# Optimization experiments

Hardware: AMD Instinct MI355X
Metric: run time of the kernel (lower is better)

Reference implementation:

```python
import jax, jax.numpy as jnp
import numpy as np

B, S, D = 4, 1024, 2048
H, KVH, HD = 32, 8, 64
N_REP = H // KVH  # 4
ROPE_THETA = 1000000.0


def _rope_tables(seq_len, head_dim, theta):
    inv_freq = 1.0 / (theta ** (np.arange(0, head_dim, 2, dtype=np.float32) / head_dim))
    t = np.arange(seq_len, dtype=np.float32)
    freqs = np.outer(t, inv_freq)                      # (S, HD/2)
    emb = np.concatenate([freqs, freqs], axis=-1)      # (S, HD)
    return jnp.asarray(np.cos(emb)), jnp.asarray(np.sin(emb))


def setup_inputs() -> dict:
    key = jax.random.key(0)
    kx, kq, kk, kv, ko = jax.random.split(key, 5)
    cos, sin = _rope_tables(S, HD, ROPE_THETA)
    s = 0.02
    return {
        "x": jax.random.normal(kx, (B, S, D), jnp.float32),
        "cos": cos,
        "sin": sin,
        "Wq": jax.random.normal(kq, (D, H * HD), jnp.float32) * s,
        "Wk": jax.random.normal(kk, (D, KVH * HD), jnp.float32) * s,
        "Wv": jax.random.normal(kv, (D, KVH * HD), jnp.float32) * s,
        "Wo": jax.random.normal(ko, (H * HD, D), jnp.float32) * s,
    }


def _rotate_half(t):
    t1, t2 = jnp.split(t, 2, axis=-1)
    return jnp.concatenate([-t2, t1], axis=-1)


def reference(x, cos, sin, Wq, Wk, Wv, Wo):
    # projections
    q = (x @ Wq).reshape(B, S, H, HD)      # (b, s, h, d)
    k = (x @ Wk).reshape(B, S, KVH, HD)
    v = (x @ Wv).reshape(B, S, KVH, HD)

    # RoPE: cos/sin (s, d) broadcast over heads (unsqueeze_dim=1 -> (s,1,d))
    c = cos[:, None, :]
    sn = sin[:, None, :]
    q = q * c + _rotate_half(q) * sn
    k = k * c + _rotate_half(k) * sn

    # GQA attention without physically repeating KV:
    # q grouped as (b, kvh, n_rep, s, d); repeat_kv '(h r)' maps q head g*n_rep+r -> kv head g
    qg = q.transpose(0, 2, 1, 3).reshape(B, KVH, N_REP, S, HD)
    kt = k.transpose(0, 2, 1, 3)  # (b, kvh, s, d)
    vt = v.transpose(0, 2, 1, 3)

    scale = 1.0 / jnp.sqrt(jnp.asarray(HD, x.dtype))
    scores = jnp.einsum('bgrqd,bgkd->bgrqk', qg, kt) * scale  # (b, kvh, rep, s, s)
    probs = jax.nn.softmax(scores, axis=-1)
    out = jnp.einsum('bgrqk,bgkd->bgrqd', probs, vt)           # (b, kvh, rep, s, d)

    out = out.reshape(B, H, S, HD).transpose(0, 2, 1, 3).reshape(B, S, H * HD)
    return out @ Wo
```

## Files before the change

kernel.cpp:

```cpp
#include <hip/hip_runtime.h>

typedef unsigned short u16;
typedef __attribute__((ext_vector_type(8))) __bf16 bf16x8;
typedef __attribute__((ext_vector_type(4))) _Float16 f16x4;
typedef __attribute__((ext_vector_type(8))) _Float16 f16x8;
typedef __attribute__((ext_vector_type(4))) float f32x4;

#define BB 4
#define SS 1024
#define DD 2048
#define HH 32
#define KVHN 8
#define HDIM 64

__device__ __forceinline__ u16 f2b(float f) {
    union { float f; unsigned u; } v; v.f = f;
    unsigned r = v.u + 0x7FFFu + ((v.u >> 16) & 1u);
    return (u16)(r >> 16);
}
__device__ __forceinline__ float b2f(u16 h) {
    union { unsigned u; float f; } v; v.u = ((unsigned)h) << 16; return v.f;
}

__device__ __forceinline__ f32x4 mfma16(bf16x8 a, bf16x8 b, f32x4 c) {
    return __builtin_amdgcn_mfma_f32_16x16x32_bf16(a, b, c, 0, 0, 0);
}
__device__ __forceinline__ f32x4 mfma16h(f16x8 a, f16x8 b, f32x4 c) {
    return __builtin_amdgcn_mfma_f32_16x16x32_f16(a, b, c, 0, 0, 0);
}

__device__ __forceinline__ void async_cp16(const void* g, void* l) {
    __builtin_amdgcn_global_load_lds((__attribute__((address_space(1))) void*)g,
                                     (__attribute__((address_space(3))) void*)l,
                                     16, 0, 0);
}

__device__ __forceinline__ void block_sync() {
    asm volatile("" ::: "memory");
    __builtin_amdgcn_s_barrier();
    asm volatile("" ::: "memory");
}

__device__ __forceinline__ f16x8 pack8_f16(const float* p) {
    union { unsigned u[4]; f16x8 v; } pu;
    pu.u[0] = __builtin_bit_cast(unsigned, __builtin_amdgcn_cvt_pkrtz(p[0], p[1]));
    pu.u[1] = __builtin_bit_cast(unsigned, __builtin_amdgcn_cvt_pkrtz(p[2], p[3]));
    pu.u[2] = __builtin_bit_cast(unsigned, __builtin_amdgcn_cvt_pkrtz(p[4], p[5]));
    pu.u[3] = __builtin_bit_cast(unsigned, __builtin_amdgcn_cvt_pkrtz(p[6], p[7]));
    return pu.v;
}

__global__ __launch_bounds__(256) void cast_x_kernel(const float* __restrict__ x,
                                                     u16* __restrict__ xb) {
    int i = (blockIdx.x * 256 + threadIdx.x) * 4;
    float4 v = *(const float4*)(x + i);
    unsigned r0 = (unsigned)f2b(v.x) | ((unsigned)f2b(v.y) << 16);
    unsigned r1 = (unsigned)f2b(v.z) | ((unsigned)f2b(v.w) << 16);
    *(uint2*)(xb + i) = make_uint2(r0, r1);
}

__global__ __launch_bounds__(256) void wtrans_all_kernel(const float* __restrict__ Wq,
                                                         const float* __restrict__ Wk,
                                                         const float* __restrict__ Wv,
                                                         const float* __restrict__ Wo,
                                                         u16* __restrict__ Wqkvt,
                                                         u16* __restrict__ Wot) {
    __shared__ float tile[32][33];
    int z = blockIdx.z;
    const float* W = (z == 0) ? Wq : (z == 1) ? Wk : (z == 2) ? Wv : Wo;
    int N = (z == 1 || z == 2) ? 512 : 2048;
    int n_off = (z == 1) ? 2048 : (z == 2) ? 2560 : 0;
    u16* Wt = (z == 3) ? Wot : Wqkvt;
    int n0 = blockIdx.x * 32;
    if (n0 >= N) return;
    int k0 = blockIdx.y * 32;
    int tid = threadIdx.x;
    int nj = tid & 31;
    int ki = tid >> 5;
#pragma unroll
    for (int it = 0; it < 4; it++) {
        int kk = it * 8 + ki;
        tile[kk][nj] = W[(size_t)(k0 + kk) * N + n0 + nj];
    }
    __syncthreads();
#pragma unroll
    for (int it = 0; it < 4; it++) {
        int nn = it * 8 + ki;
        Wt[(size_t)(n0 + nn + n_off) * 2048 + k0 + nj] = f2b(tile[nj][nn]);
    }
}

__global__ __launch_bounds__(512, 2) void gemm_qkv(const u16* __restrict__ A,
                                                   const u16* __restrict__ Bt,
                                                   u16* __restrict__ C) {
    __shared__ __align__(16) u16 Ls[2][32768];
    const int tid = threadIdx.x;
    const int lane = tid & 63;
    const int w = tid >> 6;

    const int bid = blockIdx.x;
    const int xcd = bid & 7;
    const int loc = bid >> 3;
    const int mt = (xcd & 3) * 4 + (loc & 3);
    const int nt = (xcd >> 2) * 6 + (loc >> 2);
    const int m0 = mt * 256;
    const int n0 = nt * 256;

    const int wm_h = w >> 2;
    const int wn = (w & 3) * 64;
    const int lr = lane & 15;
    const int lg = lane >> 4;

    const int sr = lane >> 3;
    const int sl = (lane & 7) ^ (sr & 7);
    const u16* pA = A + (size_t)(m0 + w * 8 + sr) * 2048 + sl * 8;
    const u16* pB = Bt + (size_t)(n0 + w * 8 + sr) * 2048 + sl * 8;

#define STA(buf_, h_, kt_)                                                               \
    {                                                                                    \
        async_cp16(pA + (size_t)((h_) * 128) * 2048 + (kt_) * 64, &Ls[buf_][(h_) * 8192 + w * 512]);            \
        async_cp16(pA + (size_t)((h_) * 128 + 64) * 2048 + (kt_) * 64, &Ls[buf_][(h_) * 8192 + 4096 + w * 512]); \
    }
#define STB(buf_, h_, kt_)                                                               \
    {                                                                                    \
        async_cp16(pB + (size_t)((h_) * 128) * 2048 + (kt_) * 64, &Ls[buf_][16384 + (h_) * 8192 + w * 512]);            \
        async_cp16(pB + (size_t)((h_) * 128 + 64) * 2048 + (kt_) * 64, &Ls[buf_][16384 + (h_) * 8192 + 4096 + w * 512]); \
    }

    f32x4 acc[8][4];
    const f32x4 zero4 = {0.f, 0.f, 0.f, 0.f};
#pragma unroll
    for (int i = 0; i < 8; i++)
#pragma unroll
        for (int j = 0; j < 4; j++) acc[i][j] = zero4;

    bf16x8 af[8], b0[4], b1[4];

#define LDA(mh_, buf_)                                                                   \
    _Pragma("unroll") for (int mi = 0; mi < 4; mi++) _Pragma("unroll") for (int ks = 0; ks < 2; ks++) { \
        int rh = (mh_) * 64 + mi * 16 + lr;                                              \
        af[mi * 2 + ks] = *(const bf16x8*)(&Ls[buf_][wm_h * 8192 + rh * 64 + (((ks * 4 + lg) ^ (lr & 7)) * 8)]); \
    }
#define LDB(dst_, nh_, buf_)                                                             \
    _Pragma("unroll") for (int ni = 0; ni < 2; ni++) _Pragma("unroll") for (int ks = 0; ks < 2; ks++) { \
        int rowb = wn + (nh_) * 32 + ni * 16 + lr;                                       \
        dst_[ni * 2 + ks] = *(const bf16x8*)(&Ls[buf_][16384 + (rowb >> 7) * 8192 + (rowb & 127) * 64 + (((ks * 4 + lg) ^ (lr & 7)) * 8)]); \
    }
#define QMM(mh_, nh_, bb_)                                                               \
    __builtin_amdgcn_s_setprio(1);                                                       \
    _Pragma("unroll") for (int mi = 0; mi < 4; mi++) _Pragma("unroll") for (int ni = 0; ni < 2; ni++) { \
        acc[(mh_) * 4 + mi][(nh_) * 2 + ni] = mfma16(af[mi * 2 + 0], bb_[ni * 2 + 0], acc[(mh_) * 4 + mi][(nh_) * 2 + ni]); \
        acc[(mh_) * 4 + mi][(nh_) * 2 + ni] = mfma16(af[mi * 2 + 1], bb_[ni * 2 + 1], acc[(mh_) * 4 + mi][(nh_) * 2 + ni]); \
    }                                                                                    \
    __builtin_amdgcn_s_setprio(0);
#define WAITLDS                                                                          \
    asm volatile("s_waitcnt lgkmcnt(0)" ::: "memory");                                   \
    __builtin_amdgcn_sched_barrier(0);

    STA(0, 0, 0); STA(0, 1, 0); STB(0, 0, 0); STB(0, 1, 0);
    STB(1, 0, 1); STB(1, 1, 1);
    asm volatile("s_waitcnt vmcnt(0)" ::: "memory");
    block_sync();

#pragma unroll 1
    for (int I = 0; I < 16; ++I) {
        const int tb = 2 * I + 1;
        const int ta2 = (2 * I + 2) & 31;
        const int tb2 = (2 * I + 3) & 31;

        LDA(0, 0); LDB(b0, 0, 0);
        STA(1, 0, tb);
        block_sync(); WAITLDS;
        QMM(0, 0, b0);
        block_sync();
        LDB(b1, 1, 0);
        STA(1, 1, tb);
        block_sync(); WAITLDS;
        QMM(0, 1, b1);
        block_sync();
        LDA(1, 0);
        STB(0, 0, ta2);
        block_sync(); WAITLDS;
        QMM(1, 1, b1);
        block_sync();
        STB(0, 1, ta2);
        block_sync(); WAITLDS;
        QMM(1, 0, b0);
        asm volatile("s_waitcnt vmcnt(4)" ::: "memory");
        block_sync();

        LDA(0, 1); LDB(b0, 0, 1);
        STA(0, 0, ta2);
        block_sync(); WAITLDS;
        QMM(0, 0, b0);
        block_sync();
        LDB(b1, 1, 1);
        STA(0, 1, ta2);
        block_sync(); WAITLDS;
        QMM(0, 1, b1);
        block_sync();
        LDA(1, 1);
        STB(1, 0, tb2);
        block_sync(); WAITLDS;
        QMM(1, 1, b1);
        block_sync();
        STB(1, 1, tb2);
        block_sync(); WAITLDS;
        QMM(1, 0, b0);
        asm volatile("s_waitcnt vmcnt(4)" ::: "memory");
        block_sync();
    }
    asm volatile("s_waitcnt vmcnt(0)" ::: "memory");

    const int lq = lg * 4;
    const int wm = wm_h * 128;
#pragma unroll
    for (int mi = 0; mi < 8; mi++)
#pragma unroll
        for (int ni = 0; ni < 4; ni++)
#pragma unroll
            for (int i = 0; i < 4; i++) {
                int r = m0 + wm + mi * 16 + lq + i;
                int c = n0 + wn + ni * 16 + lr;
                C[(size_t)r * 3072 + c] = f2b(acc[mi][ni][i]);
            }
#undef STA
#undef STB
#undef LDA
#undef LDB
#undef QMM
#undef WAITLDS
}

__global__ __launch_bounds__(512, 2) void gemm_out(const u16* __restrict__ A,
                                                   const u16* __restrict__ Bt,
                                                   float* __restrict__ C) {
    __shared__ __align__(16) u16 Ls[2][24576];
    const int tid = threadIdx.x;
    const int lane = tid & 63;
    const int w = tid >> 6;

    const int bid = blockIdx.x;
    const int xcd = bid & 7;
    const int loc = bid >> 3;
    const int mt = (xcd & 3) * 4 + (loc & 3);
    const int nt = (xcd >> 2) * 8 + (loc >> 2);
    const int m0 = mt * 256;
    const int n0 = nt * 128;

    const int wm = (w >> 2) * 128;
    const int wn = (w & 3) * 32;
    const int lr = lane & 15;
    const int lg = lane >> 4;

    const int row0 = tid >> 2;
    const int g = tid & 3;
    const int sg = g ^ ((row0 >> 1) & 3);
    const u16* pA0 = A + (size_t)(m0 + row0) * 2048 + sg * 8;
    const u16* pA1 = pA0 + (size_t)128 * 2048;
    const u16* pB0 = Bt + (size_t)(n0 + row0) * 2048 + sg * 8;

#define OSTA(buf_, ks_, T_)                                                     \
    {                                                                           \
        async_cp16(pA0 + (T_) * 64 + (ks_) * 32, &Ls[buf_][(ks_) * 8192 + w * 512]);        \
        async_cp16(pA1 + (T_) * 64 + (ks_) * 32, &Ls[buf_][(ks_) * 8192 + 4096 + w * 512]); \
    }
#define OSTB(buf_, ks_, T_)                                                     \
    {                                                                           \
        async_cp16(pB0 + (T_) * 64 + (ks_) * 32, &Ls[buf_][16384 + (ks_) * 4096 + w * 512]); \
    }

    f32x4 acc[8][2];
    const f32x4 zero4 = {0.f, 0.f, 0.f, 0.f};
#pragma unroll
    for (int i = 0; i < 8; i++)
#pragma unroll
        for (int j = 0; j < 2; j++) acc[i][j] = zero4;

    bf16x8 af[8], bfr[2];

#define OLDA(ks_)                                                               \
    _Pragma("unroll") for (int mi = 0; mi < 8; mi++) {                          \
        int r_ = wm + mi * 16 + lr;                                             \
        af[mi] = *(const bf16x8*)(&Ls[cur][(ks_) * 8192 + r_ * 32 + ((lg ^ ((r_ >> 1) & 3)) * 8)]); \
    }
#define OLDB(ks_)                                                               \
    _Pragma("unroll") for (int ni = 0; ni < 2; ni++) {                          \
        int r_ = wn + ni * 16 + lr;                                             \
        bfr[ni] = *(const bf16x8*)(&Ls[cur][16384 + (ks_) * 4096 + r_ * 32 + ((lg ^ ((r_ >> 1) & 3)) * 8)]); \
    }
#define OMM                                                                     \
    __builtin_amdgcn_s_setprio(1);                                              \
    _Pragma("unroll") for (int mi = 0; mi < 8; mi++) _Pragma("unroll") for (int ni = 0; ni < 2; ni++) { \
        acc[mi][ni] = mfma16(af[mi], bfr[ni], acc[mi][ni]);                     \
    }                                                                           \
    __builtin_amdgcn_s_setprio(0);
#define OWAITMM                                                                 \
    asm volatile("s_waitcnt lgkmcnt(0)" ::: "memory");                          \
    __builtin_amdgcn_sched_barrier(0);

    OSTA(0, 0, 0); OSTB(0, 0, 0); OSTA(0, 1, 0); OSTB(0, 1, 0);
    OSTA(1, 0, 1); OSTB(1, 0, 1);
    asm volatile("s_waitcnt vmcnt(3)" ::: "memory");
    block_sync();

#pragma unroll 2
    for (int T = 0; T < 32; ++T) {
        const int cur = T & 1;
        const int oth = cur ^ 1;
        const int Tp1 = (T + 1) & 31;
        const int Tp2 = (T + 2) & 31;

        OLDA(0); OLDB(0);
        OSTA(oth, 1, Tp1); OSTB(oth, 1, Tp1);
        block_sync(); OWAITMM;
        OMM;
        block_sync();
        OLDA(1); OLDB(1);
        OSTA(cur, 0, Tp2); OSTB(cur, 0, Tp2);
        block_sync(); OWAITMM;
        OMM;
        asm volatile("s_waitcnt vmcnt(3)" ::: "memory");
        block_sync();
    }
    asm volatile("s_waitcnt vmcnt(0)" ::: "memory");

    const int lq = lg * 4;
#pragma unroll
    for (int mi = 0; mi < 8; mi++)
#pragma unroll
        for (int ni = 0; ni < 2; ni++)
#pragma unroll
            for (int i = 0; i < 4; i++) {
                int r = m0 + wm + mi * 16 + lq + i;
                int c = n0 + wn + ni * 16 + lr;
                C[(size_t)r * 2048 + c] = acc[mi][ni][i];
            }
#undef OSTA
#undef OSTB
#undef OLDA
#undef OLDB
#undef OMM
#undef OWAITMM
}

__global__ __launch_bounds__(256) void rope_kernel(const u16* __restrict__ QKV,
                                                   const float* __restrict__ cosT,
                                                   const float* __restrict__ sinT,
                                                   u16* __restrict__ Qh,
                                                   u16* __restrict__ Kh) {
    const float QSC = 0.125f * 1.44269504088896f;
    int idx = blockIdx.x * 256 + threadIdx.x;
    int d = idx & 31;
    int t = idx >> 5;
    int hh = t % 40;
    int row = t / 40;
    int s = row & (SS - 1);
    int b = row >> 10;
    float c = cosT[s * HDIM + d];
    float sn = sinT[s * HDIM + d];
    if (hh < 32) {
        const u16* src = QKV + (size_t)row * 3072 + hh * 64 + d;
        float x1 = b2f(src[0]), x2 = b2f(src[32]);
        u16* dst = Qh + ((size_t)(b * HH + hh) * SS + s) * 64 + d;
        dst[0] = f2b((x1 * c - x2 * sn) * QSC);
        dst[32] = f2b((x2 * c + x1 * sn) * QSC);
    } else {
        int g = hh - 32;
        const u16* src = QKV + (size_t)row * 3072 + 2048 + g * 64 + d;
        float x1 = b2f(src[0]), x2 = b2f(src[32]);
        int rr = s & 7;
        int kpos = (s & ~31) + ((rr >= 4) ? 16 : 0) + ((s >> 3) & 3) * 4 + (rr & 3);
        u16* dst = Kh + ((size_t)(b * KVHN + g) * SS + kpos) * 64 + d;
        dst[0] = f2b(x1 * c - x2 * sn);
        dst[32] = f2b(x2 * c + x1 * sn);
    }
}

__global__ __launch_bounds__(256) void vtrans_kernel(const u16* __restrict__ QKV,
                                                     u16* __restrict__ Vt) {
    __shared__ u16 tile[64][65];
    int blk = blockIdx.x;
    int st = blk & 15;
    int t2 = blk >> 4;
    int g = t2 & 7;
    int b = t2 >> 3;
    int tid = threadIdx.x;
    int cj = tid & 63;
    int ri = tid >> 6;
    const u16* src = QKV + ((size_t)(b * SS + st * 64)) * 3072 + 2560 + g * 64;
#pragma unroll
    for (int it = 0; it < 16; it++) {
        int s_i = it * 4 + ri;
        tile[s_i][cj] = src[(size_t)s_i * 3072 + cj];
    }
    __syncthreads();
    u16* dst = Vt + ((size_t)(b * KVHN + g) * HDIM) * SS + st * 64;
#pragma unroll
    for (int it = 0; it < 16; it++) {
        int hd_i = it * 4 + ri;
        _Float16 hv = (_Float16)b2f(tile[cj][hd_i]);
        union { _Float16 h; u16 u; } cv; cv.h = hv;
        dst[(size_t)hd_i * SS + cj] = cv.u;
    }
}

__global__ __launch_bounds__(256, 4) void flash_kernel(const u16* __restrict__ Qh,
                                                       const u16* __restrict__ Kh,
                                                       const u16* __restrict__ Vt,
                                                       u16* __restrict__ Attn) {
    __shared__ __align__(16) u16 Kls[2][4096];
    __shared__ __align__(16) u16 Vls[2][4096];
    const int tid = threadIdx.x;
    const int lane = tid & 63;
    const int w = tid >> 6;
    const int bid = blockIdx.x;
    const int gbp = ((bid & 7) << 2) | ((bid >> 3) & 3);
    const int qt = bid >> 5;
    const int g = gbp & 7;
    const int b = gbp >> 3;
    const int h = g * 4 + w;
    const int lr = lane & 15;
    const int lg = lane >> 4;
    const int lk8 = lg * 8;
    const int lq = lg * 4;

    const u16* Qbase = Qh + ((size_t)(b * HH + h) * SS + qt * 32) * HDIM;
    bf16x8 qb[2][2];
#pragma unroll
    for (int j = 0; j < 2; j++) {
        qb[j][0] = *(const bf16x8*)(Qbase + (size_t)(j * 16 + lr) * HDIM + lk8);
        qb[j][1] = *(const bf16x8*)(Qbase + (size_t)(j * 16 + lr) * HDIM + 32 + lk8);
    }

    const u16* Kbase = Kh + (size_t)(b * KVHN + g) * SS * HDIM;
    const u16* Vbase = Vt + (size_t)(b * KVHN + g) * HDIM * SS;

    const int r0 = tid >> 3;
    const int c0 = tid & 7;

    const f32x4 zero4 = {0.f, 0.f, 0.f, 0.f};
    const f32x4 initS = {-4.f, -4.f, -4.f, -4.f};
    f32x4 o[2][4];
    float lsum[2] = {0.f, 0.f};
#pragma unroll
    for (int j = 0; j < 2; j++)
#pragma unroll
        for (int i = 0; i < 4; i++) o[j][i] = zero4;

#define STAGE(kt, p)                                                              \
    {                                                                             \
        _Pragma("unroll") for (int sh = 0; sh < 2; sh++) {                        \
            int rr = r0 + sh * 32;                                                \
            int cs = c0 ^ (rr & 7);                                              \
            async_cp16(Kbase + (size_t)((kt) + rr) * HDIM + cs * 8,               \
                       &Kls[p][sh * 2048 + w * 512]);                             \
            async_cp16(Vbase + (size_t)rr * SS + (kt) + cs * 8,                   \
                       &Vls[p][sh * 2048 + w * 512]);                             \
        }                                                                         \
    }

    STAGE(0, 0);
    __syncthreads();

    for (int t = 0; t < 16; t++) {
        const int p = t & 1;
        if (t < 15) STAGE((t + 1) * 64, p ^ 1);

#pragma unroll
        for (int c = 0; c < 2; c++) {
            f32x4 s[2][2];
#pragma unroll
            for (int halfi = 0; halfi < 2; halfi++) {
                const int R = c * 32 + halfi * 16 + lr;
                const u16* kr = &Kls[p][R * 64];
                bf16x8 kb0 = *(const bf16x8*)(kr + ((lg ^ (R & 7)) * 8));
                bf16x8 kb1 = *(const bf16x8*)(kr + (((4 + lg) ^ (R & 7)) * 8));
#pragma unroll
                for (int j = 0; j < 2; j++) {
                    f32x4 a = initS;
                    a = mfma16(kb0, qb[j][0], a);
                    a = mfma16(kb1, qb[j][1], a);
                    s[halfi][j] = a;
                }
            }

            f16x8 va[4];
#pragma unroll
            for (int hdt = 0; hdt < 4; hdt++) {
                const int R2 = hdt * 16 + lr;
                va[hdt] = *(const f16x8*)(&Vls[p][R2 * 64 + (((c * 4 + lg) ^ (R2 & 7)) * 8)]);
            }

#pragma unroll
            for (int j = 0; j < 2; j++) {
                float pv[8];
#pragma unroll
                for (int r = 0; r < 4; r++) {
                    pv[r] = __builtin_amdgcn_exp2f(s[0][j][r]);
                    pv[4 + r] = __builtin_amdgcn_exp2f(s[1][j][r]);
                }
                lsum[j] += ((pv[0] + pv[1]) + (pv[2] + pv[3])) +
                           ((pv[4] + pv[5]) + (pv[6] + pv[7]));
                f16x8 pb = pack8_f16(pv);
#pragma unroll
                for (int hdt = 0; hdt < 4; hdt++)
                    o[j][hdt] = mfma16h(va[hdt], pb, o[j][hdt]);
            }
        }
        __syncthreads();
    }

#pragma unroll
    for (int j = 0; j < 2; j++) {
        float su = lsum[j];
        su += __shfl_xor(su, 16);
        su += __shfl_xor(su, 32);
        float inv = 1.f / su;
        u16* Ob = Attn + ((size_t)(b * SS + qt * 32 + j * 16 + lr)) * 2048 + h * 64;
#pragma unroll
        for (int hdt = 0; hdt < 4; hdt++) {
            unsigned r0p = (unsigned)f2b(o[j][hdt][0] * inv) | ((unsigned)f2b(o[j][hdt][1] * inv) << 16);
            unsigned r1p = (unsigned)f2b(o[j][hdt][2] * inv) | ((unsigned)f2b(o[j][hdt][3] * inv) << 16);
            *(uint2*)(Ob + hdt * 16 + lq) = make_uint2(r0p, r1p);
        }
    }
}

extern "C" void kernel_launch(void* const* d_in, const int* in_sizes, int n_in,
                              void* d_out, int out_size, void* d_ws, size_t ws_size,
                              hipStream_t stream) {
    (void)in_sizes; (void)n_in; (void)out_size; (void)ws_size;
    const float* x = (const float*)d_in[0];
    const float* cosT = (const float*)d_in[1];
    const float* sinT = (const float*)d_in[2];
    const float* Wq = (const float*)d_in[3];
    const float* Wk = (const float*)d_in[4];
    const float* Wv = (const float*)d_in[5];
    const float* Wo = (const float*)d_in[6];
    float* out = (float*)d_out;

    char* ws = (char*)d_ws;
    u16* Xb    = (u16*)(ws);
    u16* Wqkvt = (u16*)(ws + 16777216);
    u16* Wot   = (u16*)(ws + 29360128);
    u16* QKV   = (u16*)(ws + 37748736);
    u16* Qh    = (u16*)(ws + 62914560);
    u16* Kh    = (u16*)(ws + 79691776);
    u16* Vt    = (u16*)(ws + 83886080);
    u16* Attn  = (u16*)(ws + 88080384);

    cast_x_kernel<<<8192, 256, 0, stream>>>(x, Xb);
    wtrans_all_kernel<<<dim3(64, 64, 4), 256, 0, stream>>>(Wq, Wk, Wv, Wo, Wqkvt, Wot);

    gemm_qkv<<<192, 512, 0, stream>>>(Xb, Wqkvt, QKV);

    rope_kernel<<<20480, 256, 0, stream>>>(QKV, cosT, sinT, Qh, Kh);
    vtrans_kernel<<<512, 256, 0, stream>>>(QKV, Vt);

    flash_kernel<<<1024, 256, 0, stream>>>(Qh, Kh, Vt, Attn);

    gemm_out<<<256, 512, 0, stream>>>(Attn, Wot, out);
}
```

Baseline: 272.2 us.

## Double flash query tile per block and merge prep and rope/vtrans launches

The flash attention kernel now handles 64 query rows per block instead of 32. This doubles reuse of each staged K/V tile and halves the grid. Launch bounds drop to 2 blocks per CU to fit the larger register footprint. Separately, the x cast and weight transposes are merged into one launch, and so are RoPE and the V transpose, cutting launch overhead. The risks are lower occupancy and fewer blocks to balance across CUs in the attention kernel.

```diff
diff --git a/kernel.cpp b/kernel.cpp
--- a/kernel.cpp
+++ b/kernel.cpp
@@ -50,23 +50,30 @@
     return pu.v;
 }
 
-__global__ __launch_bounds__(256) void cast_x_kernel(const float* __restrict__ x,
-                                                     u16* __restrict__ xb) {
-    int i = (blockIdx.x * 256 + threadIdx.x) * 4;
-    float4 v = *(const float4*)(x + i);
-    unsigned r0 = (unsigned)f2b(v.x) | ((unsigned)f2b(v.y) << 16);
-    unsigned r1 = (unsigned)f2b(v.z) | ((unsigned)f2b(v.w) << 16);
-    *(uint2*)(xb + i) = make_uint2(r0, r1);
-}
-
-__global__ __launch_bounds__(256) void wtrans_all_kernel(const float* __restrict__ Wq,
-                                                         const float* __restrict__ Wk,
-                                                         const float* __restrict__ Wv,
-                                                         const float* __restrict__ Wo,
-                                                         u16* __restrict__ Wqkvt,
-                                                         u16* __restrict__ Wot) {
+__global__ __launch_bounds__(256) void prep_kernel(const float* __restrict__ x,
+                                                   const float* __restrict__ Wq,
+                                                   const float* __restrict__ Wk,
+                                                   const float* __restrict__ Wv,
+                                                   const float* __restrict__ Wo,
+                                                   u16* __restrict__ xb,
+                                                   u16* __restrict__ Wqkvt,
+                                                   u16* __restrict__ Wot) {
     __shared__ float tile[32][33];
     int z = blockIdx.z;
+    int tid = threadIdx.x;
+    if (z == 4) {
+        int lb = blockIdx.y * 64 + blockIdx.x;
+        int i = (lb * 256 + tid) * 8;
+        float4 v0 = *(const float4*)(x + i);
+        float4 v1 = *(const float4*)(x + i + 4);
+        uint4 r;
+        r.x = (unsigned)f2b(v0.x) | ((unsigned)f2b(v0.y) << 16);
+        r.y = (unsigned)f2b(v0.z) | ((unsigned)f2b(v0.w) << 16);
+        r.z = (unsigned)f2b(v1.x) | ((unsigned)f2b(v1.y) << 16);
+        r.w = (unsigned)f2b(v1.z) | ((unsigned)f2b(v1.w) << 16);
+        *(uint4*)(xb + i) = r;
+        return;
+    }
     const float* W = (z == 0) ? Wq : (z == 1) ? Wk : (z == 2) ? Wv : Wo;
     int N = (z == 1 || z == 2) ? 512 : 2048;
     int n_off = (z == 1) ? 2048 : (z == 2) ? 2560 : 0;
@@ -74,7 +81,6 @@
     int n0 = blockIdx.x * 32;
     if (n0 >= N) return;
     int k0 = blockIdx.y * 32;
-    int tid = threadIdx.x;
     int nj = tid & 31;
     int ki = tid >> 5;
 #pragma unroll
@@ -173,16 +179,19 @@
         block_sync(); WAITLDS;
         QMM(0, 0, b0);
         block_sync();
+
         LDB(b1, 1, 0);
         STA(1, 1, tb);
         block_sync(); WAITLDS;
         QMM(0, 1, b1);
         block_sync();
+
         LDA(1, 0);
         STB(0, 0, ta2);
         block_sync(); WAITLDS;
         QMM(1, 1, b1);
         block_sync();
+
         STB(0, 1, ta2);
         block_sync(); WAITLDS;
         QMM(1, 0, b0);
@@ -194,16 +203,19 @@
         block_sync(); WAITLDS;
         QMM(0, 0, b0);
         block_sync();
+
         LDB(b1, 1, 1);
         STA(0, 1, ta2);
         block_sync(); WAITLDS;
         QMM(0, 1, b1);
         block_sync();
+
         LDA(1, 1);
         STB(1, 0, tb2);
         block_sync(); WAITLDS;
         QMM(1, 1, b1);
         block_sync();
+
         STB(1, 1, tb2);
         block_sync(); WAITLDS;
         QMM(1, 0, b0);
@@ -316,6 +328,7 @@
         block_sync(); OWAITMM;
         OMM;
         block_sync();
+
         OLDA(1); OLDB(1);
         OSTA(cur, 0, Tp2); OSTB(cur, 0, Tp2);
         block_sync(); OWAITMM;
@@ -344,48 +357,49 @@
 #undef OWAITMM
 }
 
-__global__ __launch_bounds__(256) void rope_kernel(const u16* __restrict__ QKV,
-                                                   const float* __restrict__ cosT,
-                                                   const float* __restrict__ sinT,
-                                                   u16* __restrict__ Qh,
-                                                   u16* __restrict__ Kh) {
-    const float QSC = 0.125f * 1.44269504088896f;
-    int idx = blockIdx.x * 256 + threadIdx.x;
-    int d = idx & 31;
-    int t = idx >> 5;
-    int hh = t % 40;
-    int row = t / 40;
-    int s = row & (SS - 1);
-    int b = row >> 10;
-    float c = cosT[s * HDIM + d];
-    float sn = sinT[s * HDIM + d];
-    if (hh < 32) {
-        const u16* src = QKV + (size_t)row * 3072 + hh * 64 + d;
-        float x1 = b2f(src[0]), x2 = b2f(src[32]);
-        u16* dst = Qh + ((size_t)(b * HH + hh) * SS + s) * 64 + d;
-        dst[0] = f2b((x1 * c - x2 * sn) * QSC);
-        dst[32] = f2b((x2 * c + x1 * sn) * QSC);
-    } else {
-        int g = hh - 32;
-        const u16* src = QKV + (size_t)row * 3072 + 2048 + g * 64 + d;
-        float x1 = b2f(src[0]), x2 = b2f(src[32]);
-        int rr = s & 7;
-        int kpos = (s & ~31) + ((rr >= 4) ? 16 : 0) + ((s >> 3) & 3) * 4 + (rr & 3);
-        u16* dst = Kh + ((size_t)(b * KVHN + g) * SS + kpos) * 64 + d;
-        dst[0] = f2b(x1 * c - x2 * sn);
-        dst[32] = f2b(x2 * c + x1 * sn);
-    }
-}
-
-__global__ __launch_bounds__(256) void vtrans_kernel(const u16* __restrict__ QKV,
+__global__ __launch_bounds__(256) void ropevt_kernel(const u16* __restrict__ QKV,
+                                                     const float* __restrict__ cosT,
+                                                     const float* __restrict__ sinT,
+                                                     u16* __restrict__ Qh,
+                                                     u16* __restrict__ Kh,
                                                      u16* __restrict__ Vt) {
     __shared__ u16 tile[64][65];
-    int blk = blockIdx.x;
+    const int bid = blockIdx.x;
+    const int tid = threadIdx.x;
+    if (bid < 20480) {
+        const float QSC = 0.125f * 1.44269504088896f;
+        int idx = bid * 256 + tid;
+        int d = idx & 31;
+        int t = idx >> 5;
+        int hh = t % 40;
+        int row = t / 40;
+        int s = row & (SS - 1);
+        int b = row >> 10;
+        float c = cosT[s * HDIM + d];
+        float sn = sinT[s * HDIM + d];
+        if (hh < 32) {
+            const u16* src = QKV + (size_t)row * 3072 + hh * 64 + d;
+            float x1 = b2f(src[0]), x2 = b2f(src[32]);
+            u16* dst = Qh + ((size_t)(b * HH + hh) * SS + s) * 64 + d;
+            dst[0] = f2b((x1 * c - x2 * sn) * QSC);
+            dst[32] = f2b((x2 * c + x1 * sn) * QSC);
+        } else {
+            int g = hh - 32;
+            const u16* src = QKV + (size_t)row * 3072 + 2048 + g * 64 + d;
+            float x1 = b2f(src[0]), x2 = b2f(src[32]);
+            int rr = s & 7;
+            int kpos = (s & ~31) + ((rr >= 4) ? 16 : 0) + ((s >> 3) & 3) * 4 + (rr & 3);
+            u16* dst = Kh + ((size_t)(b * KVHN + g) * SS + kpos) * 64 + d;
+            dst[0] = f2b(x1 * c - x2 * sn);
+            dst[32] = f2b(x2 * c + x1 * sn);
+        }
+        return;
+    }
+    int blk = bid - 20480;
     int st = blk & 15;
     int t2 = blk >> 4;
     int g = t2 & 7;
     int b = t2 >> 3;
-    int tid = threadIdx.x;
     int cj = tid & 63;
     int ri = tid >> 6;
     const u16* src = QKV + ((size_t)(b * SS + st * 64)) * 3072 + 2560 + g * 64;
@@ -405,7 +419,7 @@
     }
 }
 
-__global__ __launch_bounds__(256, 4) void flash_kernel(const u16* __restrict__ Qh,
+__global__ __launch_bounds__(256, 2) void flash_kernel(const u16* __restrict__ Qh,
                                                        const u16* __restrict__ Kh,
                                                        const u16* __restrict__ Vt,
                                                        u16* __restrict__ Attn) {
@@ -416,7 +430,7 @@
     const int w = tid >> 6;
     const int bid = blockIdx.x;
     const int gbp = ((bid & 7) << 2) | ((bid >> 3) & 3);
-    const int qt = bid >> 5;
+    const int qt2 = bid >> 5;
     const int g = gbp & 7;
     const int b = gbp >> 3;
     const int h = g * 4 + w;
@@ -425,10 +439,10 @@
     const int lk8 = lg * 8;
     const int lq = lg * 4;
 
-    const u16* Qbase = Qh + ((size_t)(b * HH + h) * SS + qt * 32) * HDIM;
-    bf16x8 qb[2][2];
-#pragma unroll
-    for (int j = 0; j < 2; j++) {
+    const u16* Qbase = Qh + ((size_t)(b * HH + h) * SS + qt2 * 64) * HDIM;
+    bf16x8 qb[4][2];
+#pragma unroll
+    for (int j = 0; j < 4; j++) {
         qb[j][0] = *(const bf16x8*)(Qbase + (size_t)(j * 16 + lr) * HDIM + lk8);
         qb[j][1] = *(const bf16x8*)(Qbase + (size_t)(j * 16 + lr) * HDIM + 32 + lk8);
     }
@@ -441,10 +455,10 @@
 
     const f32x4 zero4 = {0.f, 0.f, 0.f, 0.f};
     const f32x4 initS = {-4.f, -4.f, -4.f, -4.f};
-    f32x4 o[2][4];
-    float lsum[2] = {0.f, 0.f};
-#pragma unroll
-    for (int j = 0; j < 2; j++)
+    f32x4 o[4][4];
+    float lsum[4] = {0.f, 0.f, 0.f, 0.f};
+#pragma unroll
+    for (int j = 0; j < 4; j++)
 #pragma unroll
         for (int i = 0; i < 4; i++) o[j][i] = zero4;
 
@@ -469,7 +483,7 @@
 
 #pragma unroll
         for (int c = 0; c < 2; c++) {
-            f32x4 s[2][2];
+            f32x4 s[2][4];
 #pragma unroll
             for (int halfi = 0; halfi < 2; halfi++) {
                 const int R = c * 32 + halfi * 16 + lr;
@@ -477,7 +491,7 @@
                 bf16x8 kb0 = *(const bf16x8*)(kr + ((lg ^ (R & 7)) * 8));
                 bf16x8 kb1 = *(const bf16x8*)(kr + (((4 + lg) ^ (R & 7)) * 8));
 #pragma unroll
-                for (int j = 0; j < 2; j++) {
+                for (int j = 0; j < 4; j++) {
                     f32x4 a = initS;
                     a = mfma16(kb0, qb[j][0], a);
                     a = mfma16(kb1, qb[j][1], a);
@@ -493,7 +507,7 @@
             }
 
 #pragma unroll
-            for (int j = 0; j < 2; j++) {
+            for (int j = 0; j < 4; j++) {
                 float pv[8];
 #pragma unroll
                 for (int r = 0; r < 4; r++) {
@@ -512,12 +526,12 @@
     }
 
 #pragma unroll
-    for (int j = 0; j < 2; j++) {
+    for (int j = 0; j < 4; j++) {
         float su = lsum[j];
         su += __shfl_xor(su, 16);
         su += __shfl_xor(su, 32);
         float inv = 1.f / su;
-        u16* Ob = Attn + ((size_t)(b * SS + qt * 32 + j * 16 + lr)) * 2048 + h * 64;
+        u16* Ob = Attn + ((size_t)(b * SS + qt2 * 64 + j * 16 + lr)) * 2048 + h * 64;
 #pragma unroll
         for (int hdt = 0; hdt < 4; hdt++) {
             unsigned r0p = (unsigned)f2b(o[j][hdt][0] * inv) | ((unsigned)f2b(o[j][hdt][1] * inv) << 16);
@@ -550,15 +564,13 @@
     u16* Vt    = (u16*)(ws + 83886080);
     u16* Attn  = (u16*)(ws + 88080384);
 
-    cast_x_kernel<<<8192, 256, 0, stream>>>(x, Xb);
-    wtrans_all_kernel<<<dim3(64, 64, 4), 256, 0, stream>>>(Wq, Wk, Wv, Wo, Wqkvt, Wot);
+    prep_kernel<<<dim3(64, 64, 5), 256, 0, stream>>>(x, Wq, Wk, Wv, Wo, Xb, Wqkvt, Wot);
 
     gemm_qkv<<<192, 512, 0, stream>>>(Xb, Wqkvt, QKV);
 
-    rope_kernel<<<20480, 256, 0, stream>>>(QKV, cosT, sinT, Qh, Kh);
-    vtrans_kernel<<<512, 256, 0, stream>>>(QKV, Vt);
-
-    flash_kernel<<<1024, 256, 0, stream>>>(Qh, Kh, Vt, Attn);
+    ropevt_kernel<<<20992, 256, 0, stream>>>(QKV, cosT, sinT, Qh, Kh, Vt);
+
+    flash_kernel<<<512, 256, 0, stream>>>(Qh, Kh, Vt, Attn);
 
     gemm_out<<<256, 512, 0, stream>>>(Attn, Wot, out);
 }
```

New measurement: 258.5 us. 1.05x faster.
